# Optimization experiments

Measured on AMD Instinct MI355X. Metric: run time of the kernel, lower is better.

The kernel has to match this reference:

```python
import jax, jax.numpy as jnp
import numpy as np

# dims (see shape_source): seq S = d_t+1 must equal d_k for the unary quantum loader
B, T, D_IN = 128, 127, 48
DK = 128
S = T + 1            # tokens incl. class token; S == DK
H, L = 8, 6
P = (S * S - S) // 2  # RBS angles per head (pyramid circuit over S wires)


def _pyramid_pairs(n):
    # deterministic pyramid ordering of n(n-1)/2 adjacent-pair Givens rotations
    a, b = [], []
    for k in range(n - 1):
        for i in range(k, -1, -1):
            a.append(i)
            b.append(i + 1)
    return np.asarray(a, np.int32), np.asarray(b, np.int32)


def _build_W(phi, pa, pb, n):
    # classical simulation of the RBS pyramid circuit restricted to the unary
    # subspace: product of Givens rotations -> orthogonal n x n matrix
    def step(W, inp):
        ia, ib, th = inp
        c, s = jnp.cos(th), jnp.sin(th)
        ra, rb = W[ia], W[ib]
        W = W.at[ia].set(c * ra - s * rb)
        W = W.at[ib].set(s * ra + c * rb)
        return W, None
    W0 = jnp.eye(n, dtype=phi.dtype)
    W, _ = jax.lax.scan(step, W0, (pa, pb, phi))
    return W


def _layer_norm(x, g, b, eps=1e-5):
    m = jnp.mean(x, axis=-1, keepdims=True)
    v = jnp.mean((x - m) ** 2, axis=-1, keepdims=True)
    return (x - m) * jax.lax.rsqrt(v + eps) * g + b


def setup_inputs() -> dict:
    key = jax.random.key(0)
    ks = jax.random.split(key, 8)
    f32 = jnp.float32
    return {
        "x": jax.random.normal(ks[0], (B, T, D_IN), f32),
        "embed_w": jax.random.normal(ks[1], (DK, D_IN), f32) / np.sqrt(D_IN),
        "embed_b": jnp.zeros((DK,), f32),
        "class_token": jax.random.normal(ks[2], (DK,), f32) / DK,
        "norm0_g": jnp.ones((DK,), f32),
        "norm0_b": jnp.zeros((DK,), f32),
        "Vw": jax.random.normal(ks[3], (L, H, DK, DK), f32) / np.sqrt(DK),
        "Vb": jnp.zeros((L, H, DK), f32),
        "ln_g": jnp.ones((L, H, DK), f32),
        "ln_b": jnp.zeros((L, H, DK), f32),
        "phi": jax.random.normal(ks[4], (L, H, P), f32) / np.sqrt(S),
        "merger_w": jax.random.normal(ks[5], (L, H), f32) / np.sqrt(H),
        "merger_b": jnp.zeros((L,), f32),
    }


def reference(x, embed_w, embed_b, class_token, norm0_g, norm0_b,
              Vw, Vb, ln_g, ln_b, phi, merger_w, merger_b):
    Bsz = x.shape[0]
    pa, pb = _pyramid_pairs(S)
    # orthogonal score matrices for every (layer, head)
    Ws = jax.vmap(lambda p: _build_W(p, pa, pb, S))(phi.reshape(L * H, P))
    Ws = Ws.reshape(L, H, S, S)

    # embed patches, prepend class token (pos_embedding add is a no-op in the
    # original source: bare `+self.pos_embedding` statement, so it is omitted)
    tok = jnp.einsum('btf,df->btd', x, embed_w) + embed_b
    h = jnp.concatenate([jnp.broadcast_to(class_token, (Bsz, 1, DK)), tok], axis=1)
    h = _layer_norm(h, norm0_g, norm0_b)

    scale = 1.0 / np.sqrt(DK)
    for l in range(L):
        nrm = jnp.sqrt(jnp.sum(h * h, axis=-1))      # input3: token norms [B,S]
        u = h / nrm[..., None]                        # unit tokens (convert_array)
        hh, nn, uu = h, nrm, u

        def head(W, vw, vb, g, be):
            V = jnp.einsum('bsd,ed->bse', hh, vw) + vb
            M = jnp.einsum('bsd,de,bte->bst', uu, W, uu)
            A = (M * M) * (nn[:, :, None] * nn[:, None, :])
            Pm = jax.nn.softmax(A * scale, axis=-1)
            return _layer_norm(jnp.einsum('bst,btd->bsd', Pm, V) + hh, g, be)

        hs = jax.vmap(head)(Ws[l], Vw[l], Vb[l], ln_g[l], ln_b[l])  # [H,B,S,D]
        h = jnp.einsum('hbsd,h->bsd', hs, merger_w[l]) + merger_b[l]
    return h[:, -1, :]
```

## Files before the change

kernel.cpp:

```cpp
#include <hip/hip_runtime.h>
#include <hip/hip_bf16.h>


typedef __bf16 bf16x8 __attribute__((ext_vector_type(8)));
typedef float  f32x4  __attribute__((ext_vector_type(4)));
typedef unsigned int u32;

__device__ __forceinline__ int sidx(int row, int col)
{
    return row * 128 + ((((col >> 3) ^ (row & 15)) << 3) | (col & 7));
}

__global__ void __launch_bounds__(256)
vw_frag_kernel(const float* __restrict__ vw, __bf16* __restrict__ cvwf)
{
    const int f    = blockIdx.x * 256 + threadIdx.x;
    const int lane = f & 63;
    const int k0   = (f >> 6) & 3;
    const int t    = (f >> 8) & 7;
    const int lh   = f >> 11;
    const int row  = t * 16 + (lane & 15);
    const int col  = k0 * 32 + (lane >> 4) * 8;

    const float* src = vw + (lh * 128 + row) * 128 + col;
    __bf16* dst = cvwf + f * 8;
#pragma unroll
    for (int j = 0; j < 8; j++) dst[j] = (__bf16)src[j];
}

__global__ void __launch_bounds__(64)
sincos_kernel(const float* __restrict__ phi, float2* __restrict__ csn)
{
    const int mat = blockIdx.x / 254;
    const int t   = blockIdx.x % 254;
    const int j   = threadIdx.x;

    float th = 0.f;
    if (t < 253) {
        const int p = t & 1, i = 2 * j + p;
        const int lim = min(t, 252 - t);
        if (i <= lim) {
            const int k = (t + i) >> 1;
            th = phi[mat * 8128 + ((k * (k + 1)) >> 1) + (k - i)];
        }
    }
    float sn, cs;
    __sincosf(th, &sn, &cs);
    csn[(mat * 254 + t) * 64 + j] = make_float2(cs, sn);
}

__global__ void __launch_bounds__(64)
build_w_kernel(const float2* __restrict__ csn, __bf16* __restrict__ wt)
{
    const int mat = blockIdx.x >> 4;
    const int grp = blockIdx.x & 15;
    const int c0  = grp * 8;
    const int lam = threadIdx.x;

    const float2* base = csn + (mat * 254) * 64 + lam;

    float vlo[8], vhi[8];
#pragma unroll
    for (int j = 0; j < 8; j++) {
        vlo[j] = (2 * lam     == c0 + j) ? 1.f : 0.f;
        vhi[j] = (2 * lam + 1 == c0 + j) ? 1.f : 0.f;
    }

    float2 a  = base[0];
    float2 bq = base[64];

    for (int t = 0; t < 252; t += 2) {
        float2 c2 = base[(t + 2) * 64];
        float2 d2 = base[(t + 3) * 64];
        {
            const float cs = a.x, sn = a.y;
#pragma unroll
            for (int j = 0; j < 8; j++) {
                float lo = vlo[j], hi = vhi[j];
                vlo[j] = cs * lo - sn * hi;
                vhi[j] = sn * lo + cs * hi;
            }
        }
        {
            const float cs = bq.x, sn = bq.y;
#pragma unroll
            for (int j = 0; j < 8; j++) {
                float y  = __shfl_down(vlo[j], 1);
                float x  = vhi[j];
                float xn = cs * x - sn * y;
                float yn = sn * x + cs * y;
                vhi[j] = xn;
                float z = __shfl_up(yn, 1);
                if (lam > 0) vlo[j] = z;
            }
        }
        a = c2; bq = d2;
    }
    {
        const float cs = a.x, sn = a.y;
#pragma unroll
        for (int j = 0; j < 8; j++) {
            float lo = vlo[j], hi = vhi[j];
            vlo[j] = cs * lo - sn * hi;
            vhi[j] = sn * lo + cs * hi;
        }
    }

    u32* wtu = (u32*)wt;
#pragma unroll
    for (int j = 0; j < 8; j++) {
        __bf16 va = (__bf16)vlo[j];
        __bf16 vb = (__bf16)vhi[j];
        u32 pk = (u32)__builtin_bit_cast(unsigned short, va)
               | ((u32)__builtin_bit_cast(unsigned short, vb) << 16);
        wtu[mat * 8192 + (c0 + j) * 64 + lam] = pk;
    }
}

static __device__ __forceinline__ float block_sum_128(float v, float* sred)
{
#pragma unroll
    for (int m = 32; m; m >>= 1) v += __shfl_xor(v, m);
    __syncthreads();
    if ((threadIdx.x & 63) == 0) sred[threadIdx.x >> 6] = v;
    __syncthreads();
    return sred[0] + sred[1];
}

__global__ void __launch_bounds__(128)
embed_kernel(const float* __restrict__ x,  const float* __restrict__ ew,
             const float* __restrict__ eb, const float* __restrict__ ct,
             const float* __restrict__ g0, const float* __restrict__ b0,
             float* __restrict__ hf, __bf16* __restrict__ hb, float* __restrict__ invn)
{
    __shared__ float sx[48];
    __shared__ float sred[2];
    const int b = blockIdx.x & 127, s = blockIdx.x >> 7, d = threadIdx.x;

    float val;
    if (s == 0) {
        val = ct[d];
    } else {
        if (d < 48) sx[d] = x[(b * 127 + (s - 1)) * 48 + d];
        __syncthreads();
        float aa = 0.f;
#pragma unroll
        for (int f = 0; f < 48; f++) aa = fmaf(sx[f], ew[d * 48 + f], aa);
        val = aa + eb[d];
    }
    float mean = block_sum_128(val, sred) * (1.f / 128.f);
    float xc   = val - mean;
    float var  = block_sum_128(xc * xc, sred) * (1.f / 128.f);
    float y    = xc * rsqrtf(var + 1e-5f) * g0[d] + b0[d];
    float ss   = block_sum_128(y * y, sred);

    const int o = (b * 128 + s) * 128 + d;
    hf[o] = y;
    hb[o] = (__bf16)y;
    if (d == 0) invn[b * 128 + s] = rsqrtf(ss);
}

__global__ void __launch_bounds__(512, 4)
attn_kernel(int l,
            const float*  __restrict__ hf,  const __bf16* __restrict__ hb,
            const float*  __restrict__ invn, const __bf16* __restrict__ wt,
            const __bf16* __restrict__ vwf, const float* __restrict__ vb,
            const float* __restrict__ lng,  const float* __restrict__ lnb,
            const float* __restrict__ mwp,  __bf16* __restrict__ hs)
{
    __shared__ __align__(16) __bf16 sH[128 * 128];
    __shared__ __align__(16) __bf16 sY[128 * 128];
    __shared__ float sInv[128];
    __shared__ float sVb[128];
    __shared__ float sLg[128];
    __shared__ float sLb[128];

    const int tid  = threadIdx.x;
    const int lane = tid & 63, w = tid >> 6;
    const int l15  = lane & 15, quad = lane >> 4;
    const int b    = blockIdx.x & 127;
    const int hh   = blockIdx.x >> 7;
    const int lh   = l * 8 + hh;

    const __bf16* hbp = hb + b * 16384;
    const __bf16* wtp = wt + lh * 16384;

#pragma unroll
    for (int c = 0; c < 4; c++) {
        int ch  = tid + c * 512;
        int row = ch >> 4, cc = ch & 15;
        bf16x8 hv = *(const bf16x8*)(hbp + ch * 8);
        bf16x8 wv = *(const bf16x8*)(wtp + ch * 8);
        *(bf16x8*)(&sH[sidx(row, cc * 8)]) = hv;
        *(bf16x8*)(&sY[sidx(row, cc * 8)]) = wv;
    }
    if (tid < 128) {
        sInv[tid] = invn[b * 128 + tid];
        sVb[tid]  = vb[lh * 128 + tid];
        sLg[tid]  = lng[lh * 128 + tid];
        sLb[tid]  = lnb[lh * 128 + tid];
    }
    __syncthreads();

    const int r0 = w * 16;
    const int kq = quad * 8;
    const int q4 = quad * 4;
    const f32x4 vzero = {0.f, 0.f, 0.f, 0.f};

    f32x4 acc[8];

    auto mmL = [&](const __bf16* Ab, const __bf16* Bb) {
#pragma unroll
        for (int t = 0; t < 8; t++) acc[t] = vzero;
#pragma unroll
        for (int k0 = 0; k0 < 128; k0 += 32) {
            const int kk = k0 + kq;
            bf16x8 a0 = *(const bf16x8*)(&Ab[sidx(r0 + l15, kk)]);
#pragma unroll
            for (int t = 0; t < 8; t++) {
                bf16x8 bb = *(const bf16x8*)(&Bb[sidx(t * 16 + l15, kk)]);
                acc[t] = __builtin_amdgcn_mfma_f32_16x16x32_bf16(a0, bb, acc[t], 0, 0, 0);
            }
        }
    };

    mmL(sH, sY);
    __syncthreads();
#pragma unroll
    for (int t = 0; t < 8; t++)
#pragma unroll
        for (int r = 0; r < 4; r++)
            sY[sidx(r0 + q4 + r, t * 16 + l15)] = (__bf16)acc[t][r];

    mmL(sY, sH);

    {
        const float scale2 = 0.08838834764831843f * 1.4426950408889634f;
        float invt[8];
#pragma unroll
        for (int t = 0; t < 8; t++) invt[t] = sInv[t * 16 + l15];
        float invs[4];
#pragma unroll
        for (int r = 0; r < 4; r++) invs[r] = sInv[r0 + q4 + r];

        float mx[4] = {-3e38f, -3e38f, -3e38f, -3e38f};
#pragma unroll
        for (int t = 0; t < 8; t++)
#pragma unroll
            for (int r = 0; r < 4; r++) {
                float g = acc[t][r];
                float v = g * g * invs[r] * invt[t] * scale2;
                acc[t][r] = v;
                mx[r] = fmaxf(mx[r], v);
            }
#pragma unroll
        for (int m = 1; m < 16; m <<= 1)
#pragma unroll
            for (int r = 0; r < 4; r++) mx[r] = fmaxf(mx[r], __shfl_xor(mx[r], m));

        float sm[4] = {0.f, 0.f, 0.f, 0.f};
#pragma unroll
        for (int t = 0; t < 8; t++)
#pragma unroll
            for (int r = 0; r < 4; r++) {
                float e = exp2f(acc[t][r] - mx[r]);
                acc[t][r] = e;
                sm[r] += e;
            }
#pragma unroll
        for (int m = 1; m < 16; m <<= 1)
#pragma unroll
            for (int r = 0; r < 4; r++) sm[r] += __shfl_xor(sm[r], m);
#pragma unroll
        for (int r = 0; r < 4; r++) sm[r] = 1.0f / sm[r];
#pragma unroll
        for (int t = 0; t < 8; t++)
#pragma unroll
            for (int r = 0; r < 4; r++)
                sY[sidx(r0 + q4 + r, t * 16 + l15)] = (__bf16)(acc[t][r] * sm[r]);
    }

    float hres[8][4];
    {
        const float* hfp = hf + (b * 128 + r0 + q4) * 128;
#pragma unroll
        for (int t = 0; t < 8; t++)
#pragma unroll
            for (int r = 0; r < 4; r++)
                hres[t][r] = hfp[r * 128 + t * 16 + l15];
    }

    {
        const __bf16* vbase = vwf + (size_t)lh * 16384;
#pragma unroll
        for (int t = 0; t < 8; t++) acc[t] = vzero;
#pragma unroll
        for (int k0c = 0; k0c < 4; k0c++) {
            const int kk = k0c * 32 + kq;
            bf16x8 a0 = *(const bf16x8*)(&sH[sidx(r0 + l15, kk)]);
#pragma unroll
            for (int t = 0; t < 8; t++) {
                bf16x8 bb = *(const bf16x8*)(vbase + ((t * 4 + k0c) * 64 + lane) * 8);
                acc[t] = __builtin_amdgcn_mfma_f32_16x16x32_bf16(a0, bb, acc[t], 0, 0, 0);
            }
        }
    }
    __syncthreads();

    {
        float vbv[8];
#pragma unroll
        for (int t = 0; t < 8; t++) vbv[t] = sVb[t * 16 + l15];
#pragma unroll
        for (int t = 0; t < 8; t++)
#pragma unroll
            for (int r = 0; r < 4; r++)
                sH[sidx(t * 16 + l15, r0 + q4 + r)] = (__bf16)(acc[t][r] + vbv[t]);
    }
    __syncthreads();

    mmL(sY, sH);

    {
        const float mw = mwp[lh];
        float lgv[8], lbv[8];
#pragma unroll
        for (int t = 0; t < 8; t++) {
            lgv[t] = sLg[t * 16 + l15];
            lbv[t] = sLb[t * 16 + l15];
        }
        float sum_[4] = {0.f, 0.f, 0.f, 0.f};
        float sq_[4]  = {0.f, 0.f, 0.f, 0.f};
#pragma unroll
        for (int t = 0; t < 8; t++)
#pragma unroll
            for (int r = 0; r < 4; r++) {
                float xx = acc[t][r] + hres[t][r];
                acc[t][r] = xx;
                sum_[r] += xx;
                sq_[r]  += xx * xx;
            }
#pragma unroll
        for (int m = 1; m < 16; m <<= 1)
#pragma unroll
            for (int r = 0; r < 4; r++) {
                sum_[r] += __shfl_xor(sum_[r], m);
                sq_[r]  += __shfl_xor(sq_[r], m);
            }
        float mean[4], rstd[4];
#pragma unroll
        for (int r = 0; r < 4; r++) {
            mean[r] = sum_[r] * (1.f / 128.f);
            float var = sq_[r] * (1.f / 128.f) - mean[r] * mean[r];
            rstd[r] = rsqrtf(fmaxf(var, 0.f) + 1e-5f);
        }
        __bf16* hsp = hs + ((hh * 128 + b) * 128 + r0 + q4) * 128;
#pragma unroll
        for (int t = 0; t < 8; t++)
#pragma unroll
            for (int r = 0; r < 4; r++) {
                float y = (acc[t][r] - mean[r]) * rstd[r] * lgv[t] + lbv[t];
                hsp[r * 128 + t * 16 + l15] = (__bf16)(y * mw);
            }
    }
}

__global__ void __launch_bounds__(128)
merge_kernel(const __bf16* __restrict__ hs, const float* __restrict__ mbp, int l,
             float* __restrict__ hf, __bf16* __restrict__ hb, float* __restrict__ invn,
             float* __restrict__ out, int last)
{
    __shared__ float sred[2];
    const int b = blockIdx.x & 127, s = blockIdx.x >> 7, d = threadIdx.x;

    float acc = mbp[l];
#pragma unroll
    for (int h = 0; h < 8; h++)
        acc += (float)hs[((h * 128 + b) * 128 + s) * 128 + d];

    float ss = block_sum_128(acc * acc, sred);

    const int o = (b * 128 + s) * 128 + d;
    hf[o] = acc;
    hb[o] = (__bf16)acc;
    if (d == 0) invn[b * 128 + s] = rsqrtf(ss);
    if (last && s == 127) out[b * 128 + d] = acc;
}

extern "C" void kernel_launch(void* const* d_in, const int* in_sizes, int n_in,
                              void* d_out, int out_size, void* d_ws, size_t ws_size,
                              hipStream_t stream)
{
    (void)in_sizes; (void)n_in; (void)out_size; (void)ws_size;

    const float* x   = (const float*)d_in[0];
    const float* ew  = (const float*)d_in[1];
    const float* eb  = (const float*)d_in[2];
    const float* ct  = (const float*)d_in[3];
    const float* g0  = (const float*)d_in[4];
    const float* b0  = (const float*)d_in[5];
    const float* vw  = (const float*)d_in[6];
    const float* vb  = (const float*)d_in[7];
    const float* lng = (const float*)d_in[8];
    const float* lnb = (const float*)d_in[9];
    const float* phi = (const float*)d_in[10];
    const float* mw  = (const float*)d_in[11];
    const float* mb  = (const float*)d_in[12];
    float* out = (float*)d_out;

    char* ws = (char*)d_ws;
    __bf16* wt   = (__bf16*)(ws);
    float*  hf   = (float*)(ws + 1572864);
    __bf16* hb   = (__bf16*)(ws + 9961472);
    float*  invn = (float*)(ws + 14155776);
    __bf16* hs   = (__bf16*)(ws + 14221312);
    __bf16* cvwf = (__bf16*)(ws + 47775744);
    float2* csn  = (float2*)(ws + 49348608);

    vw_frag_kernel<<<384, 256, 0, stream>>>(vw, cvwf);
    sincos_kernel<<<48 * 254, 64, 0, stream>>>(phi, csn);
    build_w_kernel<<<768, 64, 0, stream>>>(csn, wt);
    embed_kernel<<<16384, 128, 0, stream>>>(x, ew, eb, ct, g0, b0, hf, hb, invn);
    for (int l = 0; l < 6; l++) {
        attn_kernel<<<1024, 512, 0, stream>>>(l, hf, hb, invn, wt, cvwf, vb,
                                              lng, lnb, mw, hs);
        merge_kernel<<<16384, 128, 0, stream>>>(hs, mb, l, hf, hb, invn, out,
                                                (l == 5) ? 1 : 0);
    }
}
```

Baseline: 439.5 us.

## Split W-build into more blocks and prefetch rotation coefficients in register chunks

The Givens-rotation W-builder now gives each block 4 columns instead of 8, doubling the block count to 1536 for more parallelism on a serial-latency kernel. The cos/sin table is padded to 256 steps per matrix so the rotation loop can be fully unrolled into 16 chunks of 16 coefficients, triple-buffered in registers and prefetched two chunks ahead, which hides global-load latency. The cost is more registers per thread and the padded steps (253-255) running as identity rotations with angle zero. The dependent rotation chain stays the same length, so per-block latency still bounds this kernel, which is a small part of the total time.

```diff
diff --git a/kernel.cpp b/kernel.cpp
--- a/kernel.cpp
+++ b/kernel.cpp
@@ -31,8 +31,8 @@
 __global__ void __launch_bounds__(64)
 sincos_kernel(const float* __restrict__ phi, float2* __restrict__ csn)
 {
-    const int mat = blockIdx.x / 254;
-    const int t   = blockIdx.x % 254;
+    const int mat = blockIdx.x >> 8;
+    const int t   = blockIdx.x & 255;
     const int j   = threadIdx.x;
 
     float th = 0.f;
@@ -46,69 +46,71 @@
     }
     float sn, cs;
     __sincosf(th, &sn, &cs);
-    csn[(mat * 254 + t) * 64 + j] = make_float2(cs, sn);
+    csn[(mat * 256 + t) * 64 + j] = make_float2(cs, sn);
 }
 
 __global__ void __launch_bounds__(64)
 build_w_kernel(const float2* __restrict__ csn, __bf16* __restrict__ wt)
 {
-    const int mat = blockIdx.x >> 4;
-    const int grp = blockIdx.x & 15;
-    const int c0  = grp * 8;
+    const int mat = blockIdx.x >> 5;
+    const int grp = blockIdx.x & 31;
+    const int c0  = grp * 4;
     const int lam = threadIdx.x;
 
-    const float2* base = csn + (mat * 254) * 64 + lam;
-
-    float vlo[8], vhi[8];
-#pragma unroll
-    for (int j = 0; j < 8; j++) {
+    const float2* base = csn + (mat * 256) * 64 + lam;
+
+    float vlo[4], vhi[4];
+#pragma unroll
+    for (int j = 0; j < 4; j++) {
         vlo[j] = (2 * lam     == c0 + j) ? 1.f : 0.f;
         vhi[j] = (2 * lam + 1 == c0 + j) ? 1.f : 0.f;
     }
 
-    float2 a  = base[0];
-    float2 bq = base[64];
-
-    for (int t = 0; t < 252; t += 2) {
-        float2 c2 = base[(t + 2) * 64];
-        float2 d2 = base[(t + 3) * 64];
-        {
-            const float cs = a.x, sn = a.y;
-#pragma unroll
-            for (int j = 0; j < 8; j++) {
-                float lo = vlo[j], hi = vhi[j];
-                vlo[j] = cs * lo - sn * hi;
-                vhi[j] = sn * lo + cs * hi;
-            }
-        }
-        {
-            const float cs = bq.x, sn = bq.y;
-#pragma unroll
-            for (int j = 0; j < 8; j++) {
-                float y  = __shfl_down(vlo[j], 1);
-                float x  = vhi[j];
-                float xn = cs * x - sn * y;
-                float yn = sn * x + cs * y;
-                vhi[j] = xn;
-                float z = __shfl_up(yn, 1);
-                if (lam > 0) vlo[j] = z;
-            }
-        }
-        a = c2; bq = d2;
-    }
-    {
-        const float cs = a.x, sn = a.y;
-#pragma unroll
-        for (int j = 0; j < 8; j++) {
-            float lo = vlo[j], hi = vhi[j];
-            vlo[j] = cs * lo - sn * hi;
-            vhi[j] = sn * lo + cs * hi;
+    float2 buf[3][16];
+#pragma unroll
+    for (int k = 0; k < 16; k++) buf[0][k] = base[k * 64];
+#pragma unroll
+    for (int k = 0; k < 16; k++) buf[1][k] = base[(16 + k) * 64];
+
+#pragma unroll
+    for (int g = 0; g < 16; g++) {
+        const int cb = g % 3;
+        if (g < 14) {
+            const int nb = (g + 2) % 3;
+#pragma unroll
+            for (int k = 0; k < 16; k++)
+                buf[nb][k] = base[((g + 2) * 16 + k) * 64];
+        }
+#pragma unroll
+        for (int p = 0; p < 8; p++) {
+            {
+                const float cs = buf[cb][2 * p].x, sn = buf[cb][2 * p].y;
+#pragma unroll
+                for (int j = 0; j < 4; j++) {
+                    float lo = vlo[j], hi = vhi[j];
+                    vlo[j] = cs * lo - sn * hi;
+                    vhi[j] = sn * lo + cs * hi;
+                }
+            }
+            {
+                const float cs = buf[cb][2 * p + 1].x, sn = buf[cb][2 * p + 1].y;
+#pragma unroll
+                for (int j = 0; j < 4; j++) {
+                    float y  = __shfl_down(vlo[j], 1);
+                    float x  = vhi[j];
+                    float xn = cs * x - sn * y;
+                    float yn = sn * x + cs * y;
+                    vhi[j] = xn;
+                    float z = __shfl_up(yn, 1);
+                    if (lam > 0) vlo[j] = z;
+                }
+            }
         }
     }
 
     u32* wtu = (u32*)wt;
 #pragma unroll
-    for (int j = 0; j < 8; j++) {
+    for (int j = 0; j < 4; j++) {
         __bf16 va = (__bf16)vlo[j];
         __bf16 vb = (__bf16)vhi[j];
         u32 pk = (u32)__builtin_bit_cast(unsigned short, va)
@@ -418,8 +420,8 @@
     float2* csn  = (float2*)(ws + 49348608);
 
     vw_frag_kernel<<<384, 256, 0, stream>>>(vw, cvwf);
-    sincos_kernel<<<48 * 254, 64, 0, stream>>>(phi, csn);
-    build_w_kernel<<<768, 64, 0, stream>>>(csn, wt);
+    sincos_kernel<<<48 * 256, 64, 0, stream>>>(phi, csn);
+    build_w_kernel<<<1536, 64, 0, stream>>>(csn, wt);
     embed_kernel<<<16384, 128, 0, stream>>>(x, ew, eb, ct, g0, b0, hf, hb, invn);
     for (int l = 0; l < 6; l++) {
         attn_kernel<<<1024, 512, 0, stream>>>(l, hf, hb, invn, wt, cvwf, vb,
```

Measured after the change: 427.1 us. 2.8% less time.
